# Kernel optimization log

Measured on AMD Instinct MI355X. Metric: run time of the kernel, lower is better.

Reference implementation:

```python
import jax, jax.numpy as jnp
import numpy as np

VOCAB_SIZE = 8192
NUM_MODELS = 8
STATES_PER_MODEL = 2048
ARCS_PER_STATE = 32
BATCH = 2048
MAX_BACKOFF = 4  # max backoff-chain length (bounded by n-gram order)


def setup_inputs() -> dict:
    rng = np.random.default_rng(0)
    V, M, S, K = VOCAB_SIZE, NUM_MODELS, STATES_PER_MODEL, ARCS_PER_STATE
    from_l, ilab_l, to_l = [], [], []
    for m in range(M):
        off = m * S
        # start (unigram) state: one arc per vocab label -> backoff always terminates
        f0 = np.zeros(V, dtype=np.int64)
        i0 = np.arange(V, dtype=np.int64)
        # non-start states: K arcs each, ilabels sorted within state segment
        fN = np.repeat(np.arange(1, S, dtype=np.int64), K)
        iN = np.sort(rng.integers(0, V, size=(S - 1, K)), axis=1).ravel().astype(np.int64)
        from_l.append(np.concatenate([f0, fN]) + off)
        ilab_l.append(np.concatenate([i0, iN]))
        to_l.append(rng.integers(0, S, size=V + (S - 1) * K).astype(np.int64) + off)
    from_states = np.concatenate(from_l)   # globally sorted by (state, ilabel)
    ilabels = np.concatenate(ilab_l)
    to_states = np.concatenate(to_l)
    A = from_states.shape[0]
    arcs_weights = (rng.standard_normal(A) * 0.5).astype(np.float32)
    n_states = M * S
    backoff_to = np.zeros(n_states, dtype=np.int64)
    backoff_w = (-rng.random(n_states) * 0.5).astype(np.float32)
    for m in range(M):
        off = m * S
        half = S // 2
        backoff_to[off] = off          # start state backs off to itself
        backoff_w[off] = 0.0
        backoff_to[off + 1: off + half] = off                                   # order-2 states -> start
        backoff_to[off + half: off + S] = off + rng.integers(1, half, size=S - half)  # order-3 -> order-2
    final_w = (rng.standard_normal(n_states) * 0.1).astype(np.float32)
    alpha = (0.5 + rng.random(M)).astype(np.float32)
    model_ids = rng.integers(0, M, size=BATCH).astype(np.int64)
    states = model_ids * S + rng.integers(0, S, size=BATCH)
    return {
        "all_arcs_weights": jnp.asarray(arcs_weights),
        "all_to_states": jnp.asarray(to_states),
        "all_from_states": jnp.asarray(from_states),
        "all_ilabels": jnp.asarray(ilabels),
        "all_backoff_to_states": jnp.asarray(backoff_to),
        "all_backoff_weights": jnp.asarray(backoff_w),
        "all_final_weights": jnp.asarray(final_w),
        "model2alpha": jnp.asarray(alpha),
        "states": jnp.asarray(states),
        "model_ids": jnp.asarray(model_ids),
        "eos_id": 2,
    }


def _advance(all_arcs_weights, all_backoff_weights, all_final_weights, model2alpha,
             all_to_states, all_from_states, all_ilabels, all_backoff_to_states,
             states, model_ids, eos_id):
    V = VOCAB_SIZE
    B = states.shape[0]
    A = all_from_states.shape[0]
    # arcs are contiguous per state and sorted by ilabel -> global keys are sorted
    keys = all_from_states * V + all_ilabels              # [A]
    labels = jnp.arange(V, dtype=jnp.int64)               # [V]
    cur = jnp.broadcast_to(states[:, None], (B, V))       # current state per (hyp, label)
    accum = jnp.zeros((B, V), dtype=all_arcs_weights.dtype)   # accumulated backoff weight
    scores = jnp.zeros((B, V), dtype=all_arcs_weights.dtype)
    next_states = jnp.zeros((B, V), dtype=jnp.int64)
    found = jnp.zeros((B, V), dtype=bool)
    for _ in range(MAX_BACKOFF):
        q = cur * V + labels[None, :]                     # [B, V]
        pos = jnp.searchsorted(keys, q.ravel()).reshape(B, V)
        posc = jnp.clip(pos, 0, A - 1)
        hit = (keys[posc] == q) & (~found)
        scores = jnp.where(hit, accum + all_arcs_weights[posc], scores)
        next_states = jnp.where(hit, all_to_states[posc], next_states)
        found = found | hit
        miss = ~found
        accum = accum + jnp.where(miss, all_backoff_weights[cur], jnp.zeros((), accum.dtype))
        cur = jnp.where(miss, all_backoff_to_states[cur], cur)
    alpha_b = model2alpha[model_ids]                      # [B]
    scores = scores * alpha_b[:, None]
    # eos handling: use final state weight, stay in current state
    scores = scores.at[:, eos_id].set(all_final_weights[states] * alpha_b)
    next_states = next_states.at[:, eos_id].set(states)
    return scores, next_states


def reference(all_arcs_weights, all_to_states, all_from_states, all_ilabels,
              all_backoff_to_states, all_backoff_weights, all_final_weights,
              model2alpha, states, model_ids, eos_id):
    return _advance(all_arcs_weights, all_backoff_weights, all_final_weights, model2alpha,
                    all_to_states, all_from_states, all_ilabels, all_backoff_to_states,
                    states, model_ids, eos_id)
```

## Files before the change

kernel.cpp:

```cpp
#include <hip/hip_runtime.h>

#define V    8192
#define S    2048
#define K    32
#define MAXBO 4
#define APM  (V + (S - 1) * K)

__global__ __launch_bounds__(256) void ngram_advance_kernel(
    const float* __restrict__ arc_w,
    const int*   __restrict__ to_states,
    const int*   __restrict__ ilabels,
    const int*   __restrict__ backoff_to,
    const float* __restrict__ backoff_w,
    const float* __restrict__ final_w,
    const float* __restrict__ alpha,
    const int*   __restrict__ states,
    const int*   __restrict__ model_ids,
    const int*   __restrict__ eos_id_p,
    float*       __restrict__ out,
    int B)
{
    __shared__ int   sh_lvl_state[MAXBO];
    __shared__ float sh_lvl_acc[MAXBO];
    __shared__ int   sh_nlvl;
    __shared__ int   sh_has_start;
    __shared__ float sh_start_acc;
    __shared__ float sh_alpha;
    __shared__ int   sh_m;

    const int b   = blockIdx.x;
    const int tid = threadIdx.x;

    if (tid == 0) {
        const int s0 = states[b];
        const int m  = model_ids[b];
        sh_m     = m;
        sh_alpha = alpha[m];
        float acc = 0.0f;
        int   cur = s0;
        int   n   = 0;
        int   has_start = 0;
        float sacc = 0.0f;
        for (int t = 0; t < MAXBO; ++t) {
            if ((cur % S) == 0) { has_start = 1; sacc = acc; break; }
            sh_lvl_state[n] = cur;
            sh_lvl_acc[n]   = acc;
            ++n;
            acc += backoff_w[cur];
            cur  = backoff_to[cur];
        }
        sh_nlvl      = n;
        sh_has_start = has_start;
        sh_start_acc = sacc;
    }
    __syncthreads();

    const float al = sh_alpha;
    const int   m  = sh_m;
    const long  base = (long)m * APM;
    float* scores = out + (long)b * V;
    float* nexts  = out + (long)B * V + (long)b * V;

    if (sh_has_start) {
        const float  sacc = sh_start_acc;
        const float4* w4 = (const float4*)(arc_w     + base);
        const int4*   t4 = (const int4*)  (to_states + base);
        float4* sc4 = (float4*)scores;
        float4* nx4 = (float4*)nexts;
        for (int v4 = tid; v4 < V / 4; v4 += 256) {
            const float4 w = w4[v4];
            const int4   t = t4[v4];
            float4 sc, nx;
            sc.x = (sacc + w.x) * al;  sc.y = (sacc + w.y) * al;
            sc.z = (sacc + w.z) * al;  sc.w = (sacc + w.w) * al;
            nx.x = (float)t.x;  nx.y = (float)t.y;
            nx.z = (float)t.z;  nx.w = (float)t.w;
            sc4[v4] = sc;
            nx4[v4] = nx;
        }
    } else {
        float4* sc4 = (float4*)scores;
        float4* nx4 = (float4*)nexts;
        const float4 z = make_float4(0.f, 0.f, 0.f, 0.f);
        for (int v4 = tid; v4 < V / 4; v4 += 256) { sc4[v4] = z; nx4[v4] = z; }
    }
    __syncthreads();

    for (int lvl = sh_nlvl - 1; lvl >= 0; --lvl) {
        if (tid < K) {
            const int   st  = sh_lvl_state[lvl];
            const float acc = sh_lvl_acc[lvl];
            const long abase = (long)(st / S) * APM + V + (long)((st % S) - 1) * K;
            const int il   = ilabels[abase + tid];
            const int prev = (tid > 0) ? ilabels[abase + tid - 1] : -1;
            if (il != prev) {
                scores[il] = (acc + arc_w[abase + tid]) * al;
                nexts[il]  = (float)to_states[abase + tid];
            }
        }
        __syncthreads();
    }

    if (tid == 0) {
        const int eos = *eos_id_p;
        const int s0  = states[b];
        scores[eos] = final_w[s0] * al;
        nexts[eos]  = (float)s0;
    }
}

extern "C" void kernel_launch(void* const* d_in, const int* in_sizes, int n_in,
                              void* d_out, int out_size, void* d_ws, size_t ws_size,
                              hipStream_t stream) {
    const float* arc_w      = (const float*)d_in[0];
    const int*   to_states  = (const int*)  d_in[1];
    const int*   ilabels    = (const int*)  d_in[3];
    const int*   backoff_to = (const int*)  d_in[4];
    const float* backoff_w  = (const float*)d_in[5];
    const float* final_w    = (const float*)d_in[6];
    const float* alpha      = (const float*)d_in[7];
    const int*   states     = (const int*)  d_in[8];
    const int*   model_ids  = (const int*)  d_in[9];
    const int*   eos_id_p   = (const int*)  d_in[10];

    const int B = in_sizes[8];

    ngram_advance_kernel<<<B, 256, 0, stream>>>(
        arc_w, to_states, ilabels, backoff_to, backoff_w, final_w,
        alpha, states, model_ids, eos_id_p, (float*)d_out, B);
}
```

Baseline: 30.93 us.

## Resolve backoff chain per thread and write overrides once without serialized level passes

The serial thread-0 backoff walk and the per-level barrier loop are replaced. Every thread now walks the short chain redundantly, stages each level's arcs in shared memory, prefetches the unigram row into registers, and folds the EOS value into the bulk vectorized non-temporal store. Override arcs from all levels are then written in a single pass after one barrier. Each arc checks whether a higher-priority level or the EOS already claims its label, so there are no ordered overwrites. This removes several barriers and the dependent global-load latency before the bulk write, at the cost of an O(levels*K) shared-memory duplicate scan per arc.

Measured after the change: 37.07 us. 1.2x slower.

```diff
diff --git a/kernel.cpp b/kernel.cpp
--- a/kernel.cpp
+++ b/kernel.cpp
@@ -1,12 +1,17 @@
 #include <hip/hip_runtime.h>
 
-#define V    8192
-#define S    2048
-#define K    32
+#define V     8192
+#define S     2048
+#define K     32
 #define MAXBO 4
-#define APM  (V + (S - 1) * K)
+#define APM   (V + (S - 1) * K)
+#define BLK   256
+#define NIT   (V / 4 / BLK)
 
-__global__ __launch_bounds__(256) void ngram_advance_kernel(
+typedef float f32x4 __attribute__((ext_vector_type(4)));
+typedef int   i32x4 __attribute__((ext_vector_type(4)));
+
+__global__ __launch_bounds__(BLK) void ngram_advance_kernel(
     const float* __restrict__ arc_w,
     const int*   __restrict__ to_states,
     const int*   __restrict__ ilabels,
@@ -20,92 +25,98 @@
     float*       __restrict__ out,
     int B)
 {
-    __shared__ int   sh_lvl_state[MAXBO];
-    __shared__ float sh_lvl_acc[MAXBO];
-    __shared__ int   sh_nlvl;
-    __shared__ int   sh_has_start;
-    __shared__ float sh_start_acc;
-    __shared__ float sh_alpha;
-    __shared__ int   sh_m;
+    __shared__ int   ov_il[MAXBO * K];
+    __shared__ float ov_w [MAXBO * K];
+    __shared__ float ov_t [MAXBO * K];
 
     const int b   = blockIdx.x;
     const int tid = threadIdx.x;
 
-    if (tid == 0) {
-        const int s0 = states[b];
-        const int m  = model_ids[b];
-        sh_m     = m;
-        sh_alpha = alpha[m];
-        float acc = 0.0f;
-        int   cur = s0;
-        int   n   = 0;
-        int   has_start = 0;
-        float sacc = 0.0f;
-        for (int t = 0; t < MAXBO; ++t) {
-            if ((cur % S) == 0) { has_start = 1; sacc = acc; break; }
-            sh_lvl_state[n] = cur;
-            sh_lvl_acc[n]   = acc;
-            ++n;
-            acc += backoff_w[cur];
-            cur  = backoff_to[cur];
+    const int   eos = *eos_id_p;
+    const int   s0  = states[b];
+    const int   m   = model_ids[b];
+    const float al  = alpha[m];
+    const float fw  = final_w[s0];
+
+    const long base = (long)m * APM;
+    const f32x4* w4 = (const f32x4*)(arc_w     + base);
+    const i32x4* t4 = (const i32x4*)(to_states + base);
+    f32x4 wreg[NIT];
+    i32x4 treg[NIT];
+#pragma unroll
+    for (int it = 0; it < NIT; ++it) {
+        wreg[it] = w4[tid + it * BLK];
+        treg[it] = t4[tid + it * BLK];
+    }
+
+    const int my_lvl = tid >> 5;
+    float my_acc = 0.0f;
+    int   cur = s0;
+    float acc = 0.0f;
+    int   nlvl = 0;
+    int   has_start = 0;
+    float sacc = 0.0f;
+#pragma unroll
+    for (int t = 0; t < MAXBO; ++t) {
+        if ((cur & (S - 1)) == 0) { has_start = 1; sacc = acc; break; }
+        if (t == my_lvl) my_acc = acc;
+        if (tid < K) {
+            const long abase = (long)(cur / S) * APM + V + (long)((cur & (S - 1)) - 1) * K;
+            ov_il[t * K + tid] = ilabels[abase + tid];
+            ov_w [t * K + tid] = arc_w  [abase + tid];
+            ov_t [t * K + tid] = (float)to_states[abase + tid];
         }
-        sh_nlvl      = n;
-        sh_has_start = has_start;
-        sh_start_acc = sacc;
+        ++nlvl;
+        acc += backoff_w[cur];
+        cur  = backoff_to[cur];
     }
+
+    float* scores = out + (long)b * V;
+    float* nexts  = out + (long)B * V + (long)b * V;
+    const float fsc = fw * al;
+    const float fnx = (float)s0;
+    const int eosblk  = eos >> 2;
+    const int eoslane = eos & 3;
+#pragma unroll
+    for (int it = 0; it < NIT; ++it) {
+        const int v4 = tid + it * BLK;
+        f32x4 sc, nx;
+        if (has_start) {
+            sc = (sacc + wreg[it]) * al;
+            nx = __builtin_convertvector(treg[it], f32x4);
+        } else {
+            sc = (f32x4)0.0f;
+            nx = (f32x4)0.0f;
+        }
+        if (v4 == eosblk) {
+            switch (eoslane) {
+                case 0: sc.x = fsc; nx.x = fnx; break;
+                case 1: sc.y = fsc; nx.y = fnx; break;
+                case 2: sc.z = fsc; nx.z = fnx; break;
+                default: sc.w = fsc; nx.w = fnx; break;
+            }
+        }
+        __builtin_nontemporal_store(sc, (f32x4*)scores + v4);
+        __builtin_nontemporal_store(nx, (f32x4*)nexts  + v4);
+    }
+
     __syncthreads();
 
-    const float al = sh_alpha;
-    const int   m  = sh_m;
-    const long  base = (long)m * APM;
-    float* scores = out + (long)b * V;
-    float* nexts  = out + (long)B * V + (long)b * V;
-
-    if (sh_has_start) {
-        const float  sacc = sh_start_acc;
-        const float4* w4 = (const float4*)(arc_w     + base);
-        const int4*   t4 = (const int4*)  (to_states + base);
-        float4* sc4 = (float4*)scores;
-        float4* nx4 = (float4*)nexts;
-        for (int v4 = tid; v4 < V / 4; v4 += 256) {
-            const float4 w = w4[v4];
-            const int4   t = t4[v4];
-            float4 sc, nx;
-            sc.x = (sacc + w.x) * al;  sc.y = (sacc + w.y) * al;
-            sc.z = (sacc + w.z) * al;  sc.w = (sacc + w.w) * al;
-            nx.x = (float)t.x;  nx.y = (float)t.y;
-            nx.z = (float)t.z;  nx.w = (float)t.w;
-            sc4[v4] = sc;
-            nx4[v4] = nx;
-        }
-    } else {
-        float4* sc4 = (float4*)scores;
-        float4* nx4 = (float4*)nexts;
-        const float4 z = make_float4(0.f, 0.f, 0.f, 0.f);
-        for (int v4 = tid; v4 < V / 4; v4 += 256) { sc4[v4] = z; nx4[v4] = z; }
-    }
-    __syncthreads();
-
-    for (int lvl = sh_nlvl - 1; lvl >= 0; --lvl) {
-        if (tid < K) {
-            const int   st  = sh_lvl_state[lvl];
-            const float acc = sh_lvl_acc[lvl];
-            const long abase = (long)(st / S) * APM + V + (long)((st % S) - 1) * K;
-            const int il   = ilabels[abase + tid];
-            const int prev = (tid > 0) ? ilabels[abase + tid - 1] : -1;
-            if (il != prev) {
-                scores[il] = (acc + arc_w[abase + tid]) * al;
-                nexts[il]  = (float)to_states[abase + tid];
+    if (tid < MAXBO * K) {
+        const int lvl = tid >> 5;
+        const int j   = tid & 31;
+        if (lvl < nlvl) {
+            const int il = ov_il[tid];
+            bool ok = (il != eos);
+            if (j > 0 && ov_il[tid - 1] == il) ok = false;
+            for (int pl = 0; pl < lvl; ++pl)
+                for (int q = 0; q < K; ++q)
+                    if (ov_il[pl * K + q] == il) ok = false;
+            if (ok) {
+                scores[il] = (my_acc + ov_w[tid]) * al;
+                nexts [il] = ov_t[tid];
             }
         }
-        __syncthreads();
-    }
-
-    if (tid == 0) {
-        const int eos = *eos_id_p;
-        const int s0  = states[b];
-        scores[eos] = final_w[s0] * al;
-        nexts[eos]  = (float)s0;
     }
 }
 
@@ -125,7 +136,7 @@
 
     const int B = in_sizes[8];
 
-    ngram_advance_kernel<<<B, 256, 0, stream>>>(
+    ngram_advance_kernel<<<B, BLK, 0, stream>>>(
         arc_w, to_states, ilabels, backoff_to, backoff_w, final_w,
         alpha, states, model_ids, eos_id_p, (float*)d_out, B);
 }
```
